# Kernel tuning notes

Hardware: AMD Instinct MI355X
Metric: run time of the kernel (lower is better)

The kernel has to match this reference:

```python
import jax, jax.numpy as jnp
import numpy as np

B, S, HID = 2, 2048, 4096
NH, NKV, HD = 32, 8, 128
N_REP = NH // NKV
SCALING = HD ** -0.5


def rotate_half(x):
    x1, x2 = x[..., : x.shape[-1] // 2], x[..., x.shape[-1] // 2 :]
    return jnp.concatenate((-x2, x1), axis=-1)


def setup_inputs() -> dict:
    key = jax.random.key(0)
    ks = jax.random.split(key, 8)
    hidden_states = jax.random.normal(ks[0], (B, S, HID), dtype=jnp.float32)
    # rotary embeddings (realistic cos/sin from inverse-frequency angles)
    inv_freq = 1.0 / (10000.0 ** (jnp.arange(0, HD, 2, dtype=jnp.float32) / HD))
    pos = jnp.arange(S, dtype=jnp.float32)
    ang = pos[:, None] * inv_freq[None, :]  # [S, HD/2]
    emb = jnp.concatenate([ang, ang], axis=-1)  # [S, HD]
    cos = jnp.broadcast_to(jnp.cos(emb)[None], (B, S, HD))
    sin = jnp.broadcast_to(jnp.sin(emb)[None], (B, S, HD))
    # additive causal mask [B,1,S,S]
    causal = jnp.triu(jnp.full((S, S), -1e9, dtype=jnp.float32), k=1)
    attention_mask = jnp.broadcast_to(causal[None, None], (B, 1, S, S))
    std = HID ** -0.5
    Wq = jax.random.normal(ks[1], (NH * HD, HID), dtype=jnp.float32) * std
    Wk = jax.random.normal(ks[2], (NKV * HD, HID), dtype=jnp.float32) * std
    Wv = jax.random.normal(ks[3], (NKV * HD, HID), dtype=jnp.float32) * std
    Wo = jax.random.normal(ks[4], (HID, NH * HD), dtype=jnp.float32) * std
    return {"hidden_states": hidden_states, "cos": cos, "sin": sin,
            "attention_mask": attention_mask, "Wq": Wq, "Wk": Wk, "Wv": Wv, "Wo": Wo}


def reference(hidden_states, cos, sin, attention_mask, Wq, Wk, Wv, Wo):
    b, s, _ = hidden_states.shape
    # projections (nn.Linear: x @ W.T), reshape to [B, H, S, D]
    q = (hidden_states @ Wq.T).reshape(b, s, NH, HD).transpose(0, 2, 1, 3)
    k = (hidden_states @ Wk.T).reshape(b, s, NKV, HD).transpose(0, 2, 1, 3)
    v = (hidden_states @ Wv.T).reshape(b, s, NKV, HD).transpose(0, 2, 1, 3)
    # RoPE, cos/sin broadcast over head dim
    c, sn = cos[:, None], sin[:, None]  # [B,1,S,D]
    q = q * c + rotate_half(q) * sn
    k = k * c + rotate_half(k) * sn
    # GQA repeat_kv
    k = jnp.repeat(k, N_REP, axis=1)
    v = jnp.repeat(v, N_REP, axis=1)
    # eager attention
    attn = jnp.einsum("bhqd,bhkd->bhqk", q, k) * SCALING
    attn = attn + attention_mask[:, :, :, : k.shape[2]]
    attn = jax.nn.softmax(attn.astype(jnp.float32), axis=-1).astype(q.dtype)
    out = jnp.einsum("bhqk,bhkd->bhqd", attn, v)
    out = out.transpose(0, 2, 1, 3).reshape(b, s, NH * HD)
    return out @ Wo.T
```

## Files before the change

kernel.cpp:

```cpp
#include <hip/hip_runtime.h>


typedef __bf16 bf16x8 __attribute__((ext_vector_type(8)));
typedef __bf16 bf16x4 __attribute__((ext_vector_type(4)));
typedef float floatx4 __attribute__((ext_vector_type(4)));

#define S_LEN 2048
#define HIDN  4096
#define NH    32
#define NKV   8
#define HD    128

__device__ inline void async_copy16(const void* g, void* l) {
  __builtin_amdgcn_global_load_lds(
      (const __attribute__((address_space(1))) void*)g,
      (__attribute__((address_space(3))) void*)l, 16, 0, 0);
}

__global__ __launch_bounds__(256) void cvt_bf16(const float* __restrict__ src,
                                                __bf16* __restrict__ dst, int n8)
{
  int i = blockIdx.x * 256 + threadIdx.x;
  if (i >= n8) return;
  const float4* s = (const float4*)src + (size_t)i * 2;
  float4 a = s[0], b = s[1];
  bf16x8 r = {(__bf16)a.x, (__bf16)a.y, (__bf16)a.z, (__bf16)a.w,
              (__bf16)b.x, (__bf16)b.y, (__bf16)b.z, (__bf16)b.w};
  *((bf16x8*)dst + i) = r;
}

__global__ __launch_bounds__(256) void qkv_gemm_bf16(
    const __bf16* __restrict__ A, const __bf16* __restrict__ WB,
    __bf16* __restrict__ Qb, __bf16* __restrict__ Kb, __bf16* __restrict__ Vt)
{
  __shared__ __bf16 As[128 * 32];
  __shared__ __bf16 Bs[128 * 32];
  const int tid  = threadIdx.x;
  const int wave = tid >> 6, lane = tid & 63;
  const int quad = lane >> 4, l16 = lane & 15;
  const int ln4  = lane >> 2;
  const int lc  = (((lane & 3) ^ ((lane >> 2) & 3) ^ ((lane >> 4) & 3))) * 8;
  const int swc = ((quad ^ (l16 & 3) ^ ((l16 >> 2) & 3))) * 8;
  const int wrow = (wave >> 1) * 64, wcol = (wave & 1) * 64;
  const int m0 = blockIdx.y * 128;
  const int n0 = blockIdx.x * 128;

  floatx4 acc[4][4];
  #pragma unroll
  for (int i = 0; i < 4; i++)
    #pragma unroll
    for (int j = 0; j < 4; j++) acc[i][j] = (floatx4){0.f, 0.f, 0.f, 0.f};

  for (int k0 = 0; k0 < HIDN; k0 += 32) {
    __syncthreads();
    #pragma unroll
    for (int c = 0; c < 2; ++c) {
      int ch = wave * 2 + c;
      int row = ch * 16 + ln4;
      async_copy16(A  + (size_t)(m0 + row) * HIDN + k0 + lc, &As[ch * 512 + lane * 8]);
      async_copy16(WB + (size_t)(n0 + row) * HIDN + k0 + lc, &Bs[ch * 512 + lane * 8]);
    }
    __syncthreads();

    bf16x8 af[4], bfr[4];
    #pragma unroll
    for (int i = 0; i < 4; i++)
      af[i] = *(const bf16x8*)&As[(wrow + i * 16 + l16) * 32 + swc];
    #pragma unroll
    for (int j = 0; j < 4; j++)
      bfr[j] = *(const bf16x8*)&Bs[(wcol + j * 16 + l16) * 32 + swc];
    #pragma unroll
    for (int i = 0; i < 4; i++)
      #pragma unroll
      for (int j = 0; j < 4; j++)
        acc[i][j] = __builtin_amdgcn_mfma_f32_16x16x32_bf16(bfr[j], af[i], acc[i][j], 0, 0, 0);
  }

  #pragma unroll
  for (int i = 0; i < 4; i++) {
    int m = m0 + wrow + i * 16 + l16;
    int b = m >> 11, s = m & (S_LEN - 1);
    #pragma unroll
    for (int j = 0; j < 4; j++) {
      int nb = n0 + wcol + j * 16 + quad * 4;
      if (nb < 4096) {
        int hh = nb >> 7, d = nb & 127;
        bf16x4 v = {(__bf16)acc[i][j][0], (__bf16)acc[i][j][1],
                    (__bf16)acc[i][j][2], (__bf16)acc[i][j][3]};
        *(bf16x4*)&Qb[(((size_t)b * NH + hh) * S_LEN + s) * HD + d] = v;
      } else if (nb < 5120) {
        int nl = nb - 4096, hh = nl >> 7, d = nl & 127;
        bf16x4 v = {(__bf16)acc[i][j][0], (__bf16)acc[i][j][1],
                    (__bf16)acc[i][j][2], (__bf16)acc[i][j][3]};
        *(bf16x4*)&Kb[(((size_t)b * NKV + hh) * S_LEN + s) * HD + d] = v;
      } else {
        int nl = nb - 5120, hh = nl >> 7, d = nl & 127;
        #pragma unroll
        for (int r = 0; r < 4; r++)
          Vt[(((size_t)b * NKV + hh) * HD + d + r) * S_LEN + s] = (__bf16)acc[i][j][r];
      }
    }
  }
}

__global__ __launch_bounds__(256) void out_gemm_bf16(
    const __bf16* __restrict__ A, const __bf16* __restrict__ WB,
    float* __restrict__ C)
{
  __shared__ __bf16 As[128 * 32];
  __shared__ __bf16 Bs[128 * 32];
  const int tid  = threadIdx.x;
  const int wave = tid >> 6, lane = tid & 63;
  const int quad = lane >> 4, l16 = lane & 15;
  const int ln4  = lane >> 2;
  const int lc  = (((lane & 3) ^ ((lane >> 2) & 3) ^ ((lane >> 4) & 3))) * 8;
  const int swc = ((quad ^ (l16 & 3) ^ ((l16 >> 2) & 3))) * 8;
  const int wrow = (wave >> 1) * 64, wcol = (wave & 1) * 64;
  const int m0 = blockIdx.y * 128;
  const int n0 = blockIdx.x * 128;

  floatx4 acc[4][4];
  #pragma unroll
  for (int i = 0; i < 4; i++)
    #pragma unroll
    for (int j = 0; j < 4; j++) acc[i][j] = (floatx4){0.f, 0.f, 0.f, 0.f};

  for (int k0 = 0; k0 < HIDN; k0 += 32) {
    __syncthreads();
    #pragma unroll
    for (int c = 0; c < 2; ++c) {
      int ch = wave * 2 + c;
      int row = ch * 16 + ln4;
      async_copy16(A  + (size_t)(m0 + row) * HIDN + k0 + lc, &As[ch * 512 + lane * 8]);
      async_copy16(WB + (size_t)(n0 + row) * HIDN + k0 + lc, &Bs[ch * 512 + lane * 8]);
    }
    __syncthreads();

    bf16x8 af[4], bfr[4];
    #pragma unroll
    for (int i = 0; i < 4; i++)
      af[i] = *(const bf16x8*)&As[(wrow + i * 16 + l16) * 32 + swc];
    #pragma unroll
    for (int j = 0; j < 4; j++)
      bfr[j] = *(const bf16x8*)&Bs[(wcol + j * 16 + l16) * 32 + swc];
    #pragma unroll
    for (int i = 0; i < 4; i++)
      #pragma unroll
      for (int j = 0; j < 4; j++)
        acc[i][j] = __builtin_amdgcn_mfma_f32_16x16x32_bf16(bfr[j], af[i], acc[i][j], 0, 0, 0);
  }

  #pragma unroll
  for (int i = 0; i < 4; i++) {
    int m = m0 + wrow + i * 16 + l16;
    #pragma unroll
    for (int j = 0; j < 4; j++) {
      int nb = n0 + wcol + j * 16 + quad * 4;
      *(floatx4*)&C[(size_t)m * HIDN + nb] = acc[i][j];
    }
  }
}

__global__ __launch_bounds__(256) void qkv_gemm_f32(
    const float* __restrict__ A, const float* __restrict__ Wq,
    const float* __restrict__ Wk, const float* __restrict__ Wv,
    __bf16* __restrict__ Qb, __bf16* __restrict__ Kb, __bf16* __restrict__ Vt)
{
  __shared__ __bf16 As[128 * 40];
  __shared__ __bf16 Bs[128 * 40];
  const int tid  = threadIdx.x;
  const int wave = tid >> 6, lane = tid & 63;
  const int quad = lane >> 4, l16 = lane & 15;
  const int wrow = (wave >> 1) * 64, wcol = (wave & 1) * 64;
  const int m0 = blockIdx.y * 128;
  const int n0 = blockIdx.x * 128;

  const float* W; int wr0; int sel;
  if (n0 < 4096)      { W = Wq; wr0 = n0;        sel = 0; }
  else if (n0 < 5120) { W = Wk; wr0 = n0 - 4096; sel = 1; }
  else                { W = Wv; wr0 = n0 - 5120; sel = 2; }

  floatx4 acc[4][4];
  #pragma unroll
  for (int i = 0; i < 4; i++)
    #pragma unroll
    for (int j = 0; j < 4; j++) acc[i][j] = (floatx4){0.f, 0.f, 0.f, 0.f};

  for (int k0 = 0; k0 < HIDN; k0 += 32) {
    __syncthreads();
    #pragma unroll
    for (int it = 0; it < 4; ++it) {
      int c = tid + it * 256;
      int row = c >> 3, c4 = (c & 7) * 4;
      float4 va = *(const float4*)(A + (size_t)(m0 + row) * HIDN + k0 + c4);
      __bf16* da = &As[row * 40 + c4];
      da[0] = (__bf16)va.x; da[1] = (__bf16)va.y; da[2] = (__bf16)va.z; da[3] = (__bf16)va.w;
      float4 vb = *(const float4*)(W + (size_t)(wr0 + row) * HIDN + k0 + c4);
      __bf16* db = &Bs[row * 40 + c4];
      db[0] = (__bf16)vb.x; db[1] = (__bf16)vb.y; db[2] = (__bf16)vb.z; db[3] = (__bf16)vb.w;
    }
    __syncthreads();
    bf16x8 af[4], bfr[4];
    #pragma unroll
    for (int i = 0; i < 4; i++)
      af[i] = *(const bf16x8*)&As[(wrow + i * 16 + l16) * 40 + quad * 8];
    #pragma unroll
    for (int j = 0; j < 4; j++)
      bfr[j] = *(const bf16x8*)&Bs[(wcol + j * 16 + l16) * 40 + quad * 8];
    #pragma unroll
    for (int i = 0; i < 4; i++)
      #pragma unroll
      for (int j = 0; j < 4; j++)
        acc[i][j] = __builtin_amdgcn_mfma_f32_16x16x32_bf16(af[i], bfr[j], acc[i][j], 0, 0, 0);
  }

  #pragma unroll
  for (int i = 0; i < 4; i++) {
    #pragma unroll
    for (int j = 0; j < 4; j++) {
      #pragma unroll
      for (int r = 0; r < 4; r++) {
        int m = m0 + wrow + i * 16 + quad * 4 + r;
        int n = n0 + wcol + j * 16 + l16;
        __bf16 v = (__bf16)acc[i][j][r];
        int b = m >> 11, s = m & (S_LEN - 1);
        if (sel == 0) {
          int h = n >> 7, d = n & 127;
          Qb[(((size_t)b * NH + h) * S_LEN + s) * HD + d] = v;
        } else if (sel == 1) {
          int nl = n - 4096, h = nl >> 7, d = nl & 127;
          Kb[(((size_t)b * NKV + h) * S_LEN + s) * HD + d] = v;
        } else {
          int nl = n - 5120, h = nl >> 7, d = nl & 127;
          Vt[(((size_t)b * NKV + h) * HD + d) * S_LEN + s] = v;
        }
      }
    }
  }
}

__global__ __launch_bounds__(256) void out_gemm_f32(
    const __bf16* __restrict__ A, const float* __restrict__ Wo,
    float* __restrict__ C)
{
  __shared__ __bf16 As[128 * 40];
  __shared__ __bf16 Bs[128 * 40];
  const int tid  = threadIdx.x;
  const int wave = tid >> 6, lane = tid & 63;
  const int quad = lane >> 4, l16 = lane & 15;
  const int wrow = (wave >> 1) * 64, wcol = (wave & 1) * 64;
  const int m0 = blockIdx.y * 128;
  const int n0 = blockIdx.x * 128;

  floatx4 acc[4][4];
  #pragma unroll
  for (int i = 0; i < 4; i++)
    #pragma unroll
    for (int j = 0; j < 4; j++) acc[i][j] = (floatx4){0.f, 0.f, 0.f, 0.f};

  for (int k0 = 0; k0 < HIDN; k0 += 32) {
    __syncthreads();
    #pragma unroll
    for (int it = 0; it < 2; ++it) {
      int c = tid + it * 256;
      int row = c >> 2, c8 = (c & 3) * 8;
      *(bf16x8*)&As[row * 40 + c8] =
          *(const bf16x8*)(A + (size_t)(m0 + row) * HIDN + k0 + c8);
    }
    #pragma unroll
    for (int it = 0; it < 4; ++it) {
      int c = tid + it * 256;
      int row = c >> 3, c4 = (c & 7) * 4;
      float4 vb = *(const float4*)(Wo + (size_t)(n0 + row) * HIDN + k0 + c4);
      __bf16* db = &Bs[row * 40 + c4];
      db[0] = (__bf16)vb.x; db[1] = (__bf16)vb.y; db[2] = (__bf16)vb.z; db[3] = (__bf16)vb.w;
    }
    __syncthreads();
    bf16x8 af[4], bfr[4];
    #pragma unroll
    for (int i = 0; i < 4; i++)
      af[i] = *(const bf16x8*)&As[(wrow + i * 16 + l16) * 40 + quad * 8];
    #pragma unroll
    for (int j = 0; j < 4; j++)
      bfr[j] = *(const bf16x8*)&Bs[(wcol + j * 16 + l16) * 40 + quad * 8];
    #pragma unroll
    for (int i = 0; i < 4; i++)
      #pragma unroll
      for (int j = 0; j < 4; j++)
        acc[i][j] = __builtin_amdgcn_mfma_f32_16x16x32_bf16(af[i], bfr[j], acc[i][j], 0, 0, 0);
  }

  #pragma unroll
  for (int i = 0; i < 4; i++)
    #pragma unroll
    for (int j = 0; j < 4; j++)
      #pragma unroll
      for (int r = 0; r < 4; r++) {
        int m = m0 + wrow + i * 16 + quad * 4 + r;
        int n = n0 + wcol + j * 16 + l16;
        C[(size_t)m * HIDN + n] = acc[i][j][r];
      }
}

__global__ __launch_bounds__(256) void rope_kernel(
    __bf16* __restrict__ Qb, __bf16* __restrict__ Kb,
    const float* __restrict__ cosp, const float* __restrict__ sinp)
{
  size_t i = (size_t)blockIdx.x * 256 + threadIdx.x;
  const size_t QP = (size_t)2 * NH * S_LEN * 64;
  __bf16* buf; int H; size_t t;
  if (i < QP) { buf = Qb; H = NH;  t = i; }
  else        { buf = Kb; H = NKV; t = i - QP; }
  int d = (int)(t & 63);
  int s = (int)((t >> 6) & (S_LEN - 1));
  size_t rest = t >> 17;
  int h = (int)(rest % H);
  int b = (int)(rest / H);
  size_t base = (((size_t)b * H + h) * S_LEN + s) * HD;
  float q0 = (float)buf[base + d];
  float q1 = (float)buf[base + d + 64];
  float c  = cosp[((size_t)b * S_LEN + s) * HD + d];
  float sn = sinp[((size_t)b * S_LEN + s) * HD + d];
  buf[base + d]      = (__bf16)(q0 * c - q1 * sn);
  buf[base + d + 64] = (__bf16)(q1 * c + q0 * sn);
}

__global__ __launch_bounds__(256, 2) void flash_attn(
    const __bf16* __restrict__ Q, const __bf16* __restrict__ Kc,
    const __bf16* __restrict__ Vt, __bf16* __restrict__ Out)
{
  __shared__ __bf16 Ks[64 * 136];
  __shared__ __bf16 VTs[128 * 72];
  __shared__ __bf16 Ps[4 * 32 * 72];
  const int tid  = threadIdx.x;
  const int wave = tid >> 6, lane = tid & 63;
  const int quad = lane >> 4, l16 = lane & 15;
  const int bh = blockIdx.x;
  const int h = bh & 31, b = bh >> 5;
  const int qt = 15 - (int)blockIdx.y;
  const int kvh = h >> 2;
  const size_t qbase  = (((size_t)b * NH + h) * S_LEN + qt * 128 + wave * 32) * HD;
  const size_t kbase  = ((size_t)b * NKV + kvh) * S_LEN * HD;
  const size_t vtbase = ((size_t)b * NKV + kvh) * (size_t)HD * S_LEN;
  const int psbase = wave * (32 * 72);

  bf16x8 qf[2][4];
  #pragma unroll
  for (int st = 0; st < 2; st++)
    #pragma unroll
    for (int kk = 0; kk < 4; kk++)
      qf[st][kk] = *(const bf16x8*)&Q[qbase + (size_t)(st * 16 + l16) * HD + kk * 32 + quad * 8];

  floatx4 o[2][8];
  floatx4 ol[2];
  #pragma unroll
  for (int st = 0; st < 2; st++) {
    ol[st] = (floatx4){0.f, 0.f, 0.f, 0.f};
    #pragma unroll
    for (int ct = 0; ct < 8; ct++) o[st][ct] = (floatx4){0.f, 0.f, 0.f, 0.f};
  }
  bf16x8 onesv;
  #pragma unroll
  for (int u = 0; u < 8; u++) onesv[u] = (__bf16)1.0f;

  const float c1 = 0.12753785f;
  const float c2 = -28.853900f;
  const int kj_end = 2 * qt + 2;

  bf16x8 kreg[4], vreg[4];
  #pragma unroll
  for (int it = 0; it < 4; ++it) {
    int c = tid + it * 256;
    kreg[it] = *(const bf16x8*)&Kc[kbase + (size_t)((c >> 4)) * HD + (c & 15) * 8];
    vreg[it] = *(const bf16x8*)&Vt[vtbase + (size_t)(c >> 3) * S_LEN + (c & 7) * 8];
  }

  for (int kj = 0; kj < kj_end; ++kj) {
    __syncthreads();
    #pragma unroll
    for (int it = 0; it < 4; ++it) {
      int c = tid + it * 256;
      *(bf16x8*)&Ks[(c >> 4) * 136 + (c & 15) * 8] = kreg[it];
      *(bf16x8*)&VTs[(c >> 3) * 72 + (c & 7) * 8] = vreg[it];
    }
    __syncthreads();

    if (kj + 1 < kj_end) {
      #pragma unroll
      for (int it = 0; it < 4; ++it) {
        int c = tid + it * 256;
        kreg[it] = *(const bf16x8*)&Kc[kbase + (size_t)((kj + 1) * 64 + (c >> 4)) * HD + (c & 15) * 8];
        vreg[it] = *(const bf16x8*)&Vt[vtbase + (size_t)(c >> 3) * S_LEN + (kj + 1) * 64 + (c & 7) * 8];
      }
    }

    floatx4 s[2][4];
    #pragma unroll
    for (int st = 0; st < 2; st++)
      #pragma unroll
      for (int j = 0; j < 4; j++) s[st][j] = (floatx4){0.f, 0.f, 0.f, 0.f};
    #pragma unroll
    for (int kk = 0; kk < 4; kk++) {
      bf16x8 ak[4];
      #pragma unroll
      for (int j = 0; j < 4; j++)
        ak[j] = *(const bf16x8*)&Ks[(j * 16 + l16) * 136 + kk * 32 + quad * 8];
      #pragma unroll
      for (int st = 0; st < 2; st++)
        #pragma unroll
        for (int j = 0; j < 4; j++)
          s[st][j] = __builtin_amdgcn_mfma_f32_16x16x32_bf16(ak[j], qf[st][kk], s[st][j], 0, 0, 0);
    }

    #pragma unroll
    for (int st = 0; st < 2; st++) {
      const int qrow = qt * 128 + wave * 32 + st * 16 + l16;
      #pragma unroll
      for (int j = 0; j < 4; j++) {
        const int kvb = kj * 64 + j * 16 + quad * 4;
        bf16x4 pw;
        #pragma unroll
        for (int r = 0; r < 4; r++) {
          float p = __builtin_amdgcn_exp2f(fmaf(s[st][j][r], c1, c2));
          if (kvb + r > qrow) p = 0.0f;
          pw[r] = (__bf16)p;
        }
        *(bf16x4*)&Ps[psbase + (st * 16 + l16) * 72 + j * 16 + quad * 4] = pw;
      }
    }

    #pragma unroll
    for (int kk = 0; kk < 2; kk++) {
      bf16x8 bv[8];
      #pragma unroll
      for (int ct = 0; ct < 8; ct++)
        bv[ct] = *(const bf16x8*)&VTs[(ct * 16 + l16) * 72 + kk * 32 + quad * 8];
      #pragma unroll
      for (int st = 0; st < 2; st++) {
        bf16x8 ap = *(const bf16x8*)&Ps[psbase + (st * 16 + l16) * 72 + kk * 32 + quad * 8];
        ol[st] = __builtin_amdgcn_mfma_f32_16x16x32_bf16(ap, onesv, ol[st], 0, 0, 0);
        #pragma unroll
        for (int ct = 0; ct < 8; ct++)
          o[st][ct] = __builtin_amdgcn_mfma_f32_16x16x32_bf16(ap, bv[ct], o[st][ct], 0, 0, 0);
      }
    }
  }

  #pragma unroll
  for (int st = 0; st < 2; st++) {
    #pragma unroll
    for (int r = 0; r < 4; r++) {
      float rl = 1.0f / ol[st][r];
      int qi = qt * 128 + wave * 32 + st * 16 + quad * 4 + r;
      #pragma unroll
      for (int ct = 0; ct < 8; ct++) {
        Out[((size_t)b * S_LEN + qi) * HIDN + h * HD + ct * 16 + l16] =
            (__bf16)(o[st][ct][r] * rl);
      }
    }
  }
}

extern "C" void kernel_launch(void* const* d_in, const int* in_sizes, int n_in,
                              void* d_out, int out_size, void* d_ws, size_t ws_size,
                              hipStream_t stream)
{
  const float* hs   = (const float*)d_in[0];
  const float* cosp = (const float*)d_in[1];
  const float* sinp = (const float*)d_in[2];
  const float* Wq   = (const float*)d_in[4];
  const float* Wk   = (const float*)d_in[5];
  const float* Wv   = (const float*)d_in[6];
  const float* Wo   = (const float*)d_in[7];
  float* out = (float*)d_out;

  __bf16* Qb  = (__bf16*)d_ws;
  __bf16* Kb  = Qb  + (size_t)16777216;
  __bf16* Vtb = Kb  + (size_t)4194304;

  if (ws_size >= (size_t)134217728) {
    __bf16* HSB = Vtb + (size_t)4194304;
    __bf16* AO  = HSB;
    __bf16* WB  = HSB + (size_t)16777216;

    cvt_bf16<<<8192, 256, 0, stream>>>(hs, HSB, 2097152);
    cvt_bf16<<<8192, 256, 0, stream>>>(Wq, WB, 2097152);
    cvt_bf16<<<2048, 256, 0, stream>>>(Wk, WB + 16777216, 524288);
    cvt_bf16<<<2048, 256, 0, stream>>>(Wv, WB + 20971520, 524288);
    qkv_gemm_bf16<<<dim3(48, 32), 256, 0, stream>>>(HSB, WB, Qb, Kb, Vtb);
    cvt_bf16<<<8192, 256, 0, stream>>>(Wo, WB, 2097152);
    rope_kernel<<<40960, 256, 0, stream>>>(Qb, Kb, cosp, sinp);
    flash_attn<<<dim3(64, 16), 256, 0, stream>>>(Qb, Kb, Vtb, AO);
    out_gemm_bf16<<<dim3(32, 32), 256, 0, stream>>>(AO, WB, out);
  } else {
    __bf16* AO = Vtb + (size_t)4194304;
    qkv_gemm_f32<<<dim3(48, 32), 256, 0, stream>>>(hs, Wq, Wk, Wv, Qb, Kb, Vtb);
    rope_kernel<<<40960, 256, 0, stream>>>(Qb, Kb, cosp, sinp);
    flash_attn<<<dim3(64, 16), 256, 0, stream>>>(Qb, Kb, Vtb, AO);
    out_gemm_f32<<<dim3(32, 32), 256, 0, stream>>>(AO, Wo, out);
  }
}
```

Measured before the change: 787.1 us.

## Rewrite bf16 GEMMs with 4-stage async LDS pipeline and larger 512-thread tiles

Replaces the single-buffered, double-barrier QKV and output GEMM loops with a shared templated core. The core keeps four LDS stages in flight using global_load_lds, waits on explicit vmcnt counts, and issues one barrier per k-step. Tiles grow to 128x256 for QKV and 256x256 for the output projection, with 512-thread blocks, a new XOR swizzle and s_setprio around the MFMA block. The aim is to hide global-load latency and raise data reuse per block. In exchange it uses more LDS and registers, and correctness depends on the vmcnt accounting matching the number of loads issued per stage.

```diff
diff --git a/kernel.cpp b/kernel.cpp
--- a/kernel.cpp
+++ b/kernel.cpp
@@ -15,6 +15,15 @@
   __builtin_amdgcn_global_load_lds(
       (const __attribute__((address_space(1))) void*)g,
       (__attribute__((address_space(3))) void*)l, 16, 0, 0);
+}
+
+template<int N> __device__ __forceinline__ void waitv() {
+  static_assert(N == 0 || N == 3 || N == 4 || N == 6 || N == 8, "vmcnt");
+  if constexpr (N == 0)      asm volatile("s_waitcnt vmcnt(0)" ::: "memory");
+  else if constexpr (N == 3) asm volatile("s_waitcnt vmcnt(3)" ::: "memory");
+  else if constexpr (N == 4) asm volatile("s_waitcnt vmcnt(4)" ::: "memory");
+  else if constexpr (N == 6) asm volatile("s_waitcnt vmcnt(6)" ::: "memory");
+  else                       asm volatile("s_waitcnt vmcnt(8)" ::: "memory");
 }
 
 __global__ __launch_bounds__(256) void cvt_bf16(const float* __restrict__ src,
@@ -29,134 +38,149 @@
   *((bf16x8*)dst + i) = r;
 }
 
-__global__ __launch_bounds__(256) void qkv_gemm_bf16(
+template<int MI_REP>
+__device__ __forceinline__ void gemm_core(
+    const __bf16* __restrict__ A, const __bf16* __restrict__ WB,
+    __bf16* lds, int m0, int n0, int tid, floatx4 (&acc)[MI_REP][4])
+{
+  constexpr int BM       = MI_REP * 32;
+  constexpr int A_BYTES  = BM * 64;
+  constexpr int STAGE_B  = A_BYTES + 256 * 64;
+  constexpr int A_ROUNDS = BM / 128;
+  constexpr int LPT      = A_ROUNDS + 2;
+  constexpr int NK       = HIDN / 32;
+
+  const int wave = tid >> 6, lane = tid & 63;
+  const int quad = lane >> 4, l16 = lane & 15;
+  const int wm = wave >> 2, wn = wave & 3;
+
+  size_t a_src[A_ROUNDS], b_src[2];
+  #pragma unroll
+  for (int ra = 0; ra < A_ROUNDS; ra++) {
+    int idx = ra * 512 + tid;
+    int row = idx >> 2, qlog = (idx & 3) ^ ((idx >> 3) & 3);
+    a_src[ra] = (size_t)(m0 + row) * HIDN + qlog * 8;
+  }
+  #pragma unroll
+  for (int rb = 0; rb < 2; rb++) {
+    int idx = rb * 512 + tid;
+    int row = idx >> 2, qlog = (idx & 3) ^ ((idx >> 3) & 3);
+    b_src[rb] = (size_t)(n0 + row) * HIDN + qlog * 8;
+  }
+  const int sw   = (quad ^ ((l16 >> 1) & 3)) * 16;
+  const int a_rd = (wm * (MI_REP * 16) + l16) * 64 + sw;
+  const int b_rd = A_BYTES + (wn * 64 + l16) * 64 + sw;
+
+  #pragma unroll
+  for (int mi = 0; mi < MI_REP; mi++)
+    #pragma unroll
+    for (int ni = 0; ni < 4; ni++) acc[mi][ni] = (floatx4){0.f, 0.f, 0.f, 0.f};
+
+  char* ldsb = (char*)lds;
+  auto stage = [&](int kt) {
+    char* sb = ldsb + (size_t)(kt & 3) * STAGE_B;
+    const __bf16* ak = A  + (size_t)kt * 32;
+    const __bf16* bk = WB + (size_t)kt * 32;
+    #pragma unroll
+    for (int ra = 0; ra < A_ROUNDS; ra++)
+      async_copy16(ak + a_src[ra], sb + (ra * 512 + tid) * 16);
+    #pragma unroll
+    for (int rb = 0; rb < 2; rb++)
+      async_copy16(bk + b_src[rb], sb + A_BYTES + (rb * 512 + tid) * 16);
+  };
+
+  stage(0); stage(1); stage(2);
+
+  #pragma unroll 4
+  for (int kt = 0; kt < NK; kt++) {
+    if (kt < NK - 2)       waitv<2 * LPT>();
+    else if (kt == NK - 2) waitv<LPT>();
+    else                   waitv<0>();
+    __builtin_amdgcn_s_barrier();
+    asm volatile("" ::: "memory");
+    if (kt + 3 < NK) stage(kt + 3);
+
+    const char* sb = ldsb + (size_t)(kt & 3) * STAGE_B;
+    bf16x8 bv[4], av[MI_REP];
+    #pragma unroll
+    for (int ni = 0; ni < 4; ni++)
+      bv[ni] = *(const bf16x8*)(sb + b_rd + ni * 1024);
+    #pragma unroll
+    for (int mi = 0; mi < MI_REP; mi++)
+      av[mi] = *(const bf16x8*)(sb + a_rd + mi * 1024);
+
+    __builtin_amdgcn_s_setprio(1);
+    #pragma unroll
+    for (int mi = 0; mi < MI_REP; mi++)
+      #pragma unroll
+      for (int ni = 0; ni < 4; ni++)
+        acc[mi][ni] = __builtin_amdgcn_mfma_f32_16x16x32_bf16(
+            bv[ni], av[mi], acc[mi][ni], 0, 0, 0);
+    __builtin_amdgcn_s_setprio(0);
+  }
+}
+
+__global__ __launch_bounds__(512, 2) void qkv_gemm_bf16(
     const __bf16* __restrict__ A, const __bf16* __restrict__ WB,
     __bf16* __restrict__ Qb, __bf16* __restrict__ Kb, __bf16* __restrict__ Vt)
 {
-  __shared__ __bf16 As[128 * 32];
-  __shared__ __bf16 Bs[128 * 32];
-  const int tid  = threadIdx.x;
+  __shared__ __bf16 lds[4 * (128 + 256) * 32];
+  const int tid = threadIdx.x;
+  const int m0 = blockIdx.y * 128, n0 = blockIdx.x * 256;
+  floatx4 acc[4][4];
+  gemm_core<4>(A, WB, lds, m0, n0, tid, acc);
+
   const int wave = tid >> 6, lane = tid & 63;
   const int quad = lane >> 4, l16 = lane & 15;
-  const int ln4  = lane >> 2;
-  const int lc  = (((lane & 3) ^ ((lane >> 2) & 3) ^ ((lane >> 4) & 3))) * 8;
-  const int swc = ((quad ^ (l16 & 3) ^ ((l16 >> 2) & 3))) * 8;
-  const int wrow = (wave >> 1) * 64, wcol = (wave & 1) * 64;
-  const int m0 = blockIdx.y * 128;
-  const int n0 = blockIdx.x * 128;
-
-  floatx4 acc[4][4];
-  #pragma unroll
-  for (int i = 0; i < 4; i++)
-    #pragma unroll
-    for (int j = 0; j < 4; j++) acc[i][j] = (floatx4){0.f, 0.f, 0.f, 0.f};
-
-  for (int k0 = 0; k0 < HIDN; k0 += 32) {
-    __syncthreads();
-    #pragma unroll
-    for (int c = 0; c < 2; ++c) {
-      int ch = wave * 2 + c;
-      int row = ch * 16 + ln4;
-      async_copy16(A  + (size_t)(m0 + row) * HIDN + k0 + lc, &As[ch * 512 + lane * 8]);
-      async_copy16(WB + (size_t)(n0 + row) * HIDN + k0 + lc, &Bs[ch * 512 + lane * 8]);
-    }
-    __syncthreads();
-
-    bf16x8 af[4], bfr[4];
-    #pragma unroll
-    for (int i = 0; i < 4; i++)
-      af[i] = *(const bf16x8*)&As[(wrow + i * 16 + l16) * 32 + swc];
-    #pragma unroll
-    for (int j = 0; j < 4; j++)
-      bfr[j] = *(const bf16x8*)&Bs[(wcol + j * 16 + l16) * 32 + swc];
-    #pragma unroll
-    for (int i = 0; i < 4; i++)
-      #pragma unroll
-      for (int j = 0; j < 4; j++)
-        acc[i][j] = __builtin_amdgcn_mfma_f32_16x16x32_bf16(bfr[j], af[i], acc[i][j], 0, 0, 0);
-  }
-
-  #pragma unroll
-  for (int i = 0; i < 4; i++) {
-    int m = m0 + wrow + i * 16 + l16;
+  const int wm = wave >> 2, wn = wave & 3;
+  #pragma unroll
+  for (int mi = 0; mi < 4; mi++) {
+    int m = m0 + wm * 64 + mi * 16 + l16;
     int b = m >> 11, s = m & (S_LEN - 1);
     #pragma unroll
-    for (int j = 0; j < 4; j++) {
-      int nb = n0 + wcol + j * 16 + quad * 4;
+    for (int ni = 0; ni < 4; ni++) {
+      int nb = n0 + wn * 64 + ni * 16 + quad * 4;
       if (nb < 4096) {
         int hh = nb >> 7, d = nb & 127;
-        bf16x4 v = {(__bf16)acc[i][j][0], (__bf16)acc[i][j][1],
-                    (__bf16)acc[i][j][2], (__bf16)acc[i][j][3]};
+        bf16x4 v = {(__bf16)acc[mi][ni][0], (__bf16)acc[mi][ni][1],
+                    (__bf16)acc[mi][ni][2], (__bf16)acc[mi][ni][3]};
         *(bf16x4*)&Qb[(((size_t)b * NH + hh) * S_LEN + s) * HD + d] = v;
       } else if (nb < 5120) {
         int nl = nb - 4096, hh = nl >> 7, d = nl & 127;
-        bf16x4 v = {(__bf16)acc[i][j][0], (__bf16)acc[i][j][1],
-                    (__bf16)acc[i][j][2], (__bf16)acc[i][j][3]};
+        bf16x4 v = {(__bf16)acc[mi][ni][0], (__bf16)acc[mi][ni][1],
+                    (__bf16)acc[mi][ni][2], (__bf16)acc[mi][ni][3]};
         *(bf16x4*)&Kb[(((size_t)b * NKV + hh) * S_LEN + s) * HD + d] = v;
       } else {
         int nl = nb - 5120, hh = nl >> 7, d = nl & 127;
         #pragma unroll
         for (int r = 0; r < 4; r++)
-          Vt[(((size_t)b * NKV + hh) * HD + d + r) * S_LEN + s] = (__bf16)acc[i][j][r];
-      }
-    }
-  }
-}
-
-__global__ __launch_bounds__(256) void out_gemm_bf16(
+          Vt[(((size_t)b * NKV + hh) * HD + d + r) * S_LEN + s] =
+              (__bf16)acc[mi][ni][r];
+      }
+    }
+  }
+}
+
+__global__ __launch_bounds__(512, 2) void out_gemm_bf16(
     const __bf16* __restrict__ A, const __bf16* __restrict__ WB,
     float* __restrict__ C)
 {
-  __shared__ __bf16 As[128 * 32];
-  __shared__ __bf16 Bs[128 * 32];
-  const int tid  = threadIdx.x;
+  __shared__ __bf16 lds[4 * (256 + 256) * 32];
+  const int tid = threadIdx.x;
+  const int m0 = blockIdx.y * 256, n0 = blockIdx.x * 256;
+  floatx4 acc[8][4];
+  gemm_core<8>(A, WB, lds, m0, n0, tid, acc);
+
   const int wave = tid >> 6, lane = tid & 63;
   const int quad = lane >> 4, l16 = lane & 15;
-  const int ln4  = lane >> 2;
-  const int lc  = (((lane & 3) ^ ((lane >> 2) & 3) ^ ((lane >> 4) & 3))) * 8;
-  const int swc = ((quad ^ (l16 & 3) ^ ((l16 >> 2) & 3))) * 8;
-  const int wrow = (wave >> 1) * 64, wcol = (wave & 1) * 64;
-  const int m0 = blockIdx.y * 128;
-  const int n0 = blockIdx.x * 128;
-
-  floatx4 acc[4][4];
-  #pragma unroll
-  for (int i = 0; i < 4; i++)
-    #pragma unroll
-    for (int j = 0; j < 4; j++) acc[i][j] = (floatx4){0.f, 0.f, 0.f, 0.f};
-
-  for (int k0 = 0; k0 < HIDN; k0 += 32) {
-    __syncthreads();
-    #pragma unroll
-    for (int c = 0; c < 2; ++c) {
-      int ch = wave * 2 + c;
-      int row = ch * 16 + ln4;
-      async_copy16(A  + (size_t)(m0 + row) * HIDN + k0 + lc, &As[ch * 512 + lane * 8]);
-      async_copy16(WB + (size_t)(n0 + row) * HIDN + k0 + lc, &Bs[ch * 512 + lane * 8]);
-    }
-    __syncthreads();
-
-    bf16x8 af[4], bfr[4];
-    #pragma unroll
-    for (int i = 0; i < 4; i++)
-      af[i] = *(const bf16x8*)&As[(wrow + i * 16 + l16) * 32 + swc];
-    #pragma unroll
-    for (int j = 0; j < 4; j++)
-      bfr[j] = *(const bf16x8*)&Bs[(wcol + j * 16 + l16) * 32 + swc];
-    #pragma unroll
-    for (int i = 0; i < 4; i++)
-      #pragma unroll
-      for (int j = 0; j < 4; j++)
-        acc[i][j] = __builtin_amdgcn_mfma_f32_16x16x32_bf16(bfr[j], af[i], acc[i][j], 0, 0, 0);
-  }
-
-  #pragma unroll
-  for (int i = 0; i < 4; i++) {
-    int m = m0 + wrow + i * 16 + l16;
-    #pragma unroll
-    for (int j = 0; j < 4; j++) {
-      int nb = n0 + wcol + j * 16 + quad * 4;
-      *(floatx4*)&C[(size_t)m * HIDN + nb] = acc[i][j];
+  const int wm = wave >> 2, wn = wave & 3;
+  #pragma unroll
+  for (int mi = 0; mi < 8; mi++) {
+    int m = m0 + wm * 128 + mi * 16 + l16;
+    #pragma unroll
+    for (int ni = 0; ni < 4; ni++) {
+      int nb = n0 + wn * 64 + ni * 16 + quad * 4;
+      *(floatx4*)&C[(size_t)m * HIDN + nb] = acc[mi][ni];
     }
   }
 }
@@ -487,11 +511,11 @@
     cvt_bf16<<<8192, 256, 0, stream>>>(Wq, WB, 2097152);
     cvt_bf16<<<2048, 256, 0, stream>>>(Wk, WB + 16777216, 524288);
     cvt_bf16<<<2048, 256, 0, stream>>>(Wv, WB + 20971520, 524288);
-    qkv_gemm_bf16<<<dim3(48, 32), 256, 0, stream>>>(HSB, WB, Qb, Kb, Vtb);
+    qkv_gemm_bf16<<<dim3(24, 32), 512, 0, stream>>>(HSB, WB, Qb, Kb, Vtb);
     cvt_bf16<<<8192, 256, 0, stream>>>(Wo, WB, 2097152);
     rope_kernel<<<40960, 256, 0, stream>>>(Qb, Kb, cosp, sinp);
     flash_attn<<<dim3(64, 16), 256, 0, stream>>>(Qb, Kb, Vtb, AO);
-    out_gemm_bf16<<<dim3(32, 32), 256, 0, stream>>>(AO, WB, out);
+    out_gemm_bf16<<<dim3(16, 16), 512, 0, stream>>>(AO, WB, out);
   } else {
     __bf16* AO = Vtb + (size_t)4194304;
     qkv_gemm_f32<<<dim3(48, 32), 256, 0, stream>>>(hs, Wq, Wk, Wv, Qb, Kb, Vtb);
```

New measurement: 672.9 us. -14.5%, faster.
